# Kernel tuning notes

Hardware: AMD Instinct MI355X
Metric: run time of the kernel (lower is better)

Reference implementation:

```python
import jax, jax.numpy as jnp
import numpy as np

NEG = -1e9


def setup_inputs() -> dict:
    key = jax.random.key(0)
    ks = jax.random.split(key, 5)
    B, N, D = 2, 1024, 40
    x = jax.random.normal(ks[0], (B, N, D), dtype=jnp.float32)
    # Linear(2D->D): store as (2D, D) so y = cat @ W1 + b1 (transposed torch layout)
    W1 = jax.random.normal(ks[1], (2 * D, D), dtype=jnp.float32) * (1.0 / np.sqrt(2 * D))
    b1 = jax.random.normal(ks[2], (D,), dtype=jnp.float32) * 0.01
    W2 = jax.random.normal(ks[3], (D, D), dtype=jnp.float32) * (1.0 / np.sqrt(D))
    b2 = jax.random.normal(ks[4], (D,), dtype=jnp.float32) * 0.01
    return {"x": x, "W1": W1, "b1": b1, "W2": W2, "b2": b2}


def reference(x, W1, b1, W2, b2):
    B, N, D = x.shape
    # cat([xi, xj]) @ W1 == xi @ W1[:D] + xj @ W1[D:] -> avoid (B,N,N,2D) materialization
    ai = x @ W1[:D]          # (B, N, D), contribution of row index i
    aj = x @ W1[D:]          # (B, N, D), contribution of col index j
    h = jax.nn.gelu(ai[:, :, None, :] + aj[:, None, :, :] + b1, approximate=False)  # (B,N,N,D)
    p = h @ W2 + b2          # (B, N, N, D)
    mask = jnp.triu(jnp.ones((N, N), dtype=bool), 1)  # True where j > i (masked out)
    p = jnp.where(mask[None, :, :, None], 0.0, p)
    sq = jnp.sum(p * p, axis=-1)                       # (B, N, N)
    s = jnp.sqrt(jnp.where(mask[None], 1.0, sq))       # safe sqrt at masked zeros
    s = jnp.where(mask[None], NEG, s)
    w = jax.nn.softmax(s, axis=-1)                     # softmax over j
    return jnp.sum(w[..., None] * p, axis=2)           # (B, N, D)
```

## Files before the change

kernel.cpp:

```cpp
#include <hip/hip_runtime.h>
#include <math.h>

#define D 40
#define NN 1024
#define BB 2

typedef __attribute__((ext_vector_type(8))) _Float16 f16x8;
typedef __attribute__((ext_vector_type(4))) float f32x4;

__device__ __forceinline__ unsigned int pk16(float a, float b) {
    return __builtin_bit_cast(unsigned int, __builtin_amdgcn_cvt_pkrtz(a, b));
}

__device__ __forceinline__ float gelu_tanh(float a) {
    float u = a * a;
    float t1 = fmaf(0.10294366f, u, 2.3022083f);
    float e = __builtin_amdgcn_exp2f(a * t1);
    float r = __builtin_amdgcn_rcpf(e + 1.0f);
    return fmaf(-a, r, a);
}

__device__ __forceinline__ void pinf(float& x) { asm volatile("" : "+v"(x)); }
__device__ __forceinline__ void pin4(float4& v) {
    asm volatile("" : "+v"(v.x), "+v"(v.y), "+v"(v.z), "+v"(v.w));
}
__device__ __forceinline__ void pin8(f16x8& v) {
    uint4 u = __builtin_bit_cast(uint4, v);
    asm volatile("" : "+v"(u.x), "+v"(u.y), "+v"(u.z), "+v"(u.w));
    v = __builtin_bit_cast(f16x8, u);
}

__device__ __forceinline__ f16x8 frag8(float4 a0, float4 a1, float4 x0, float4 x1) {
    float g0 = gelu_tanh(a0.x + x0.x);
    float g1 = gelu_tanh(a0.y + x0.y);
    float g2 = gelu_tanh(a0.z + x0.z);
    float g3 = gelu_tanh(a0.w + x0.w);
    float g4 = gelu_tanh(a1.x + x1.x);
    float g5 = gelu_tanh(a1.y + x1.y);
    float g6 = gelu_tanh(a1.z + x1.z);
    float g7 = gelu_tanh(a1.w + x1.w);
    return __builtin_bit_cast(f16x8,
        make_uint4(pk16(g0, g1), pk16(g2, g3), pk16(g4, g5), pk16(g6, g7)));
}

__global__ __launch_bounds__(256) void precompute_kernel(
    const float* __restrict__ x, const float* __restrict__ W1,
    const float* __restrict__ b1, const float* __restrict__ W2,
    float* __restrict__ ai, float* __restrict__ aj, uint4* __restrict__ w2fT) {
    const int t = threadIdx.x;
    const int bid = blockIdx.x;
    const int r = (bid << 1) + (t >> 7);
    const int tl = t & 127;
    const float* xr = x + (size_t)r * D;

    if (tl < D) {
        const int d = tl;
        float s = b1[d];
#pragma unroll
        for (int k = 0; k < D; ++k) s = fmaf(xr[k], W1[k * D + d], s);
        ai[(size_t)r * D + d] = s;
    } else if (tl >= 64 && tl < 64 + D) {
        const int d = tl - 64;
        float s = 0.0f;
#pragma unroll
        for (int k = 0; k < D; ++k) s = fmaf(xr[k], W1[(D + k) * D + d], s);
        aj[(size_t)r * D + d] = s;
    }

    if (bid == 0 && t < 64) {
        const int lr = t & 15, lg = t >> 4;
#pragma unroll
        for (int mt = 0; mt < 3; ++mt)
#pragma unroll
            for (int kt = 0; kt < 2; ++kt) {
                unsigned int u[4];
#pragma unroll
                for (int pe = 0; pe < 4; ++pe) {
                    int k0 = kt * 32 + lg * 8 + pe * 2;
                    int dd = mt * 16 + lr;
                    float v0 = (k0 < D && dd < D) ? W2[k0 * D + dd] : 0.0f;
                    float v1 = (k0 + 1 < D && dd < D) ? W2[(k0 + 1) * D + dd] : 0.0f;
                    u[pe] = pk16(v0, v1);
                }
                w2fT[(mt * 2 + kt) * 64 + t] = make_uint4(u[0], u[1], u[2], u[3]);
            }
    }
}

__global__ __launch_bounds__(256)
__attribute__((amdgpu_waves_per_eu(4)))
void pair_kernel(
    const float* __restrict__ ai_g, const float* __restrict__ aj_g,
    const uint4* __restrict__ w2fT, const float* __restrict__ b2,
    float* __restrict__ out) {
    __shared__ float mbuf[224];

    const int t = threadIdx.x;
    const int bid = blockIdx.x;
    const int bb = bid & 1;
    const int i = NN - 1 - (bid >> 1);
    const int w = t >> 6;
    const int l = t & 63;
    const int lr = l & 15;
    const int lg = l >> 4;

    f16x8 w2t[3][2];
#pragma unroll
    for (int mt = 0; mt < 3; ++mt)
#pragma unroll
        for (int kt = 0; kt < 2; ++kt) {
            w2t[mt][kt] = __builtin_bit_cast(f16x8, w2fT[(mt * 2 + kt) * 64 + l]);
            pin8(w2t[mt][kt]);
        }

    float bv2[3][4];
#pragma unroll
    for (int mt = 0; mt < 3; ++mt)
#pragma unroll
        for (int r = 0; r < 4; ++r) {
            int d = mt * 16 + lg * 4 + r;
            bv2[mt][r] = (d < D) ? b2[d] : 0.0f;
            pinf(bv2[mt][r]);
        }

    const float* ai_row = ai_g + ((size_t)bb * NN + i) * D;
    float4 air0 = *reinterpret_cast<const float4*>(ai_row + (lg << 3));
    float4 air1 = *reinterpret_cast<const float4*>(ai_row + (lg << 3) + 4);
    float4 ai32 = *reinterpret_cast<const float4*>(ai_row + 32 + ((l >> 5) << 2));
    pin4(air0); pin4(air1); pin4(ai32);

    const float* aj_b = aj_g + (size_t)bb * NN * D;

    float m_run = 0.0f, l_run = 0.0f;
    float o[3][4];
#pragma unroll
    for (int mt = 0; mt < 3; ++mt)
#pragma unroll
        for (int r = 0; r < 4; ++r) o[mt][r] = 0.0f;

    const int idxA = lr << 2;

    auto window = [&](int jbase, float4 qa0, float4 qa1, float4 qb0,
                      float4 qb1, float4 qt, bool masked) {
        unsigned int pd0, pd1;
        {
            float g0 = gelu_tanh(ai32.x + qt.x);
            float g1 = gelu_tanh(ai32.y + qt.y);
            float g2 = gelu_tanh(ai32.z + qt.z);
            float g3 = gelu_tanh(ai32.w + qt.w);
            pd0 = pk16(g0, g1);
            pd1 = pk16(g2, g3);
        }
        uint4 tB0, tB1;
        tB0.x = __builtin_amdgcn_ds_bpermute(idxA,       pd0);
        tB0.y = __builtin_amdgcn_ds_bpermute(idxA,       pd1);
        tB0.z = __builtin_amdgcn_ds_bpermute(idxA + 128, pd0);
        tB0.w = __builtin_amdgcn_ds_bpermute(idxA + 128, pd1);
        tB1.x = __builtin_amdgcn_ds_bpermute(idxA + 64,  pd0);
        tB1.y = __builtin_amdgcn_ds_bpermute(idxA + 64,  pd1);
        tB1.z = __builtin_amdgcn_ds_bpermute(idxA + 192, pd0);
        tB1.w = __builtin_amdgcn_ds_bpermute(idxA + 192, pd1);

        f32x4 acc[3][2];
#pragma unroll
        for (int mt = 0; mt < 3; ++mt)
#pragma unroll
            for (int n = 0; n < 2; ++n)
                acc[mt][n] = (f32x4){bv2[mt][0], bv2[mt][1], bv2[mt][2], bv2[mt][3]};
        {
            f16x8 B = frag8(air0, air1, qa0, qa1);
            f16x8 Bt = __builtin_bit_cast(f16x8, tB0);
#pragma unroll
            for (int mt = 0; mt < 3; ++mt) {
                acc[mt][0] = __builtin_amdgcn_mfma_f32_16x16x32_f16(
                    w2t[mt][0], B, acc[mt][0], 0, 0, 0);
                acc[mt][0] = __builtin_amdgcn_mfma_f32_16x16x32_f16(
                    w2t[mt][1], Bt, acc[mt][0], 0, 0, 0);
            }
        }
        {
            f16x8 B = frag8(air0, air1, qb0, qb1);
            f16x8 Bt = __builtin_bit_cast(f16x8, tB1);
#pragma unroll
            for (int mt = 0; mt < 3; ++mt) {
                acc[mt][1] = __builtin_amdgcn_mfma_f32_16x16x32_f16(
                    w2t[mt][0], B, acc[mt][1], 0, 0, 0);
                acc[mt][1] = __builtin_amdgcn_mfma_f32_16x16x32_f16(
                    w2t[mt][1], Bt, acc[mt][1], 0, 0, 0);
            }
        }

        float sv[2];
#pragma unroll
        for (int n = 0; n < 2; ++n) {
            float sq = 0.0f;
#pragma unroll
            for (int mt = 0; mt < 3; ++mt)
#pragma unroll
                for (int r = 0; r < 4; ++r)
                    sq = fmaf(acc[mt][n][r], acc[mt][n][r], sq);
            sq += __shfl_xor(sq, 16);
            sq += __shfl_xor(sq, 32);
            if (masked) {
                int j = jbase + n * 16 + lr;
                sv[n] = (j <= i) ? __builtin_amdgcn_sqrtf(sq) : -1e30f;
            } else {
                sv[n] = __builtin_amdgcn_sqrtf(sq);
            }
        }
        float mx = fmaxf(sv[0], sv[1]);
        mx = fmaxf(mx, __shfl_xor(mx, 1));
        mx = fmaxf(mx, __shfl_xor(mx, 2));
        mx = fmaxf(mx, __shfl_xor(mx, 4));
        mx = fmaxf(mx, __shfl_xor(mx, 8));
        if (mx > m_run) {
            float scale = __expf(m_run - mx);
            l_run *= scale;
#pragma unroll
            for (int mt = 0; mt < 3; ++mt)
#pragma unroll
                for (int r = 0; r < 4; ++r) o[mt][r] *= scale;
            m_run = mx;
        }
        float w0 = __expf(sv[0] - m_run);
        float w1 = __expf(sv[1] - m_run);
        l_run += w0 + w1;
#pragma unroll
        for (int mt = 0; mt < 3; ++mt)
#pragma unroll
            for (int r = 0; r < 4; ++r)
                o[mt][r] = fmaf(w0, acc[mt][0][r], fmaf(w1, acc[mt][1][r], o[mt][r]));
    };

    int jbase = w << 5;
    const float* pA = aj_b + (size_t)(jbase + lr) * D + (lg << 3);
    const float* pT = aj_b + (size_t)(jbase + (l & 31)) * D + 32 + ((l >> 5) << 2);
    for (; jbase + 31 <= i; jbase += 128) {
        float4 qa0 = *reinterpret_cast<const float4*>(pA);
        float4 qa1 = *reinterpret_cast<const float4*>(pA + 4);
        float4 qb0 = *reinterpret_cast<const float4*>(pA + 16 * D);
        float4 qb1 = *reinterpret_cast<const float4*>(pA + 16 * D + 4);
        float4 qt  = *reinterpret_cast<const float4*>(pT);
        pA += 128 * D;
        pT += 128 * D;
        window(jbase, qa0, qa1, qb0, qb1, qt, false);
    }
    if (jbase <= i) {
        const int j0 = min(jbase + lr, i);
        const int j1 = min(jbase + 16 + lr, i);
        const int jt = min(jbase + (l & 31), i);
        const float* r0 = aj_b + (size_t)j0 * D + (lg << 3);
        const float* r1 = aj_b + (size_t)j1 * D + (lg << 3);
        float4 qa0 = *reinterpret_cast<const float4*>(r0);
        float4 qa1 = *reinterpret_cast<const float4*>(r0 + 4);
        float4 qb0 = *reinterpret_cast<const float4*>(r1);
        float4 qb1 = *reinterpret_cast<const float4*>(r1 + 4);
        float4 qt  = *reinterpret_cast<const float4*>(
            aj_b + (size_t)jt * D + 32 + ((l >> 5) << 2));
        window(jbase, qa0, qa1, qb0, qb1, qt, true);
    }

#pragma unroll
    for (int mt = 0; mt < 3; ++mt)
#pragma unroll
        for (int r = 0; r < 4; ++r) {
            float v = o[mt][r];
            v += __shfl_xor(v, 1);
            v += __shfl_xor(v, 2);
            v += __shfl_xor(v, 4);
            v += __shfl_xor(v, 8);
            o[mt][r] = v;
        }
    l_run += __shfl_xor(l_run, 1);
    l_run += __shfl_xor(l_run, 2);
    l_run += __shfl_xor(l_run, 4);
    l_run += __shfl_xor(l_run, 8);

    if (lr == 0) {
#pragma unroll
        for (int mt = 0; mt < 3; ++mt)
#pragma unroll
            for (int r = 0; r < 4; ++r) {
                int d = mt * 16 + lg * 4 + r;
                if (d < D) mbuf[w * 56 + d] = o[mt][r];
            }
        if (lg == 0) { mbuf[w * 56 + 48] = l_run; mbuf[w * 56 + 49] = m_run; }
    }
    __syncthreads();
    if (t < D) {
        float Mg = fmaxf(fmaxf(mbuf[49], mbuf[56 + 49]),
                         fmaxf(mbuf[112 + 49], mbuf[168 + 49]));
        float L = 0.0f, val = 0.0f;
#pragma unroll
        for (int ww = 0; ww < 4; ++ww) {
            float c = __expf(mbuf[ww * 56 + 49] - Mg);
            L = fmaf(c, mbuf[ww * 56 + 48], L);
            val = fmaf(c, mbuf[ww * 56 + t], val);
        }
        out[((size_t)bb * NN + i) * D + t] = val / L;
    }
}

extern "C" void kernel_launch(void* const* d_in, const int* in_sizes, int n_in,
                              void* d_out, int out_size, void* d_ws, size_t ws_size,
                              hipStream_t stream) {
    const float* x  = (const float*)d_in[0];
    const float* W1 = (const float*)d_in[1];
    const float* b1 = (const float*)d_in[2];
    const float* W2 = (const float*)d_in[3];
    const float* b2 = (const float*)d_in[4];
    float* out = (float*)d_out;

    float* ai = (float*)d_ws;
    float* aj = ai + (size_t)BB * NN * D;
    uint4* w2fT = (uint4*)(aj + (size_t)BB * NN * D);

    precompute_kernel<<<BB * NN / 2, 256, 0, stream>>>(x, W1, b1, W2, ai, aj, w2fT);
    pair_kernel<<<BB * NN, 256, 0, stream>>>(ai, aj, w2fT, b2, out);
}
```

Before: 34.90 us.

## Split pair work into balanced fixed-size tasks with partial sums and merge kernel

```diff
diff --git a/kernel.cpp b/kernel.cpp
--- a/kernel.cpp
+++ b/kernel.cpp
@@ -4,6 +4,11 @@
 #define D 40
 #define NN 1024
 #define BB 2
+#define NWPB 4608
+#define NTASK (2*NWPB)
+#define GP 1024
+#define TPB 9
+#define PSTR 44
 
 typedef __attribute__((ext_vector_type(8))) _Float16 f16x8;
 typedef __attribute__((ext_vector_type(4))) float f32x4;
@@ -18,16 +23,6 @@
     float e = __builtin_amdgcn_exp2f(a * t1);
     float r = __builtin_amdgcn_rcpf(e + 1.0f);
     return fmaf(-a, r, a);
-}
-
-__device__ __forceinline__ void pinf(float& x) { asm volatile("" : "+v"(x)); }
-__device__ __forceinline__ void pin4(float4& v) {
-    asm volatile("" : "+v"(v.x), "+v"(v.y), "+v"(v.z), "+v"(v.w));
-}
-__device__ __forceinline__ void pin8(f16x8& v) {
-    uint4 u = __builtin_bit_cast(uint4, v);
-    asm volatile("" : "+v"(u.x), "+v"(u.y), "+v"(u.z), "+v"(u.w));
-    v = __builtin_bit_cast(f16x8, u);
 }
 
 __device__ __forceinline__ f16x8 frag8(float4 a0, float4 a1, float4 x0, float4 x1) {
@@ -87,31 +82,26 @@
     }
 }
 
-__global__ __launch_bounds__(256)
-__attribute__((amdgpu_waves_per_eu(4)))
-void pair_kernel(
+__global__ __launch_bounds__(256) void pair_partial_kernel(
     const float* __restrict__ ai_g, const float* __restrict__ aj_g,
     const uint4* __restrict__ w2fT, const float* __restrict__ b2,
-    float* __restrict__ out) {
+    float* __restrict__ partial) {
     __shared__ float mbuf[224];
 
     const int t = threadIdx.x;
     const int bid = blockIdx.x;
-    const int bb = bid & 1;
-    const int i = NN - 1 - (bid >> 1);
-    const int w = t >> 6;
+    const int wv = t >> 6;
     const int l = t & 63;
     const int lr = l & 15;
     const int lg = l >> 4;
+    const int idxA = lr << 2;
 
     f16x8 w2t[3][2];
 #pragma unroll
     for (int mt = 0; mt < 3; ++mt)
 #pragma unroll
-        for (int kt = 0; kt < 2; ++kt) {
+        for (int kt = 0; kt < 2; ++kt)
             w2t[mt][kt] = __builtin_bit_cast(f16x8, w2fT[(mt * 2 + kt) * 64 + l]);
-            pin8(w2t[mt][kt]);
-        }
 
     float bv2[3][4];
 #pragma unroll
@@ -120,184 +110,191 @@
         for (int r = 0; r < 4; ++r) {
             int d = mt * 16 + lg * 4 + r;
             bv2[mt][r] = (d < D) ? b2[d] : 0.0f;
-            pinf(bv2[mt][r]);
-        }
-
-    const float* ai_row = ai_g + ((size_t)bb * NN + i) * D;
-    float4 air0 = *reinterpret_cast<const float4*>(ai_row + (lg << 3));
-    float4 air1 = *reinterpret_cast<const float4*>(ai_row + (lg << 3) + 4);
-    float4 ai32 = *reinterpret_cast<const float4*>(ai_row + 32 + ((l >> 5) << 2));
-    pin4(air0); pin4(air1); pin4(ai32);
-
-    const float* aj_b = aj_g + (size_t)bb * NN * D;
-
-    float m_run = 0.0f, l_run = 0.0f;
-    float o[3][4];
-#pragma unroll
-    for (int mt = 0; mt < 3; ++mt)
-#pragma unroll
-        for (int r = 0; r < 4; ++r) o[mt][r] = 0.0f;
-
-    const int idxA = lr << 2;
-
-    auto window = [&](int jbase, float4 qa0, float4 qa1, float4 qb0,
-                      float4 qb1, float4 qt, bool masked) {
-        unsigned int pd0, pd1;
-        {
-            float g0 = gelu_tanh(ai32.x + qt.x);
-            float g1 = gelu_tanh(ai32.y + qt.y);
-            float g2 = gelu_tanh(ai32.z + qt.z);
-            float g3 = gelu_tanh(ai32.w + qt.w);
-            pd0 = pk16(g0, g1);
-            pd1 = pk16(g2, g3);
-        }
-        uint4 tB0, tB1;
-        tB0.x = __builtin_amdgcn_ds_bpermute(idxA,       pd0);
-        tB0.y = __builtin_amdgcn_ds_bpermute(idxA,       pd1);
-        tB0.z = __builtin_amdgcn_ds_bpermute(idxA + 128, pd0);
-        tB0.w = __builtin_amdgcn_ds_bpermute(idxA + 128, pd1);
-        tB1.x = __builtin_amdgcn_ds_bpermute(idxA + 64,  pd0);
-        tB1.y = __builtin_amdgcn_ds_bpermute(idxA + 64,  pd1);
-        tB1.z = __builtin_amdgcn_ds_bpermute(idxA + 192, pd0);
-        tB1.w = __builtin_amdgcn_ds_bpermute(idxA + 192, pd1);
-
-        f32x4 acc[3][2];
+        }
+
+    int T0 = bid * TPB;
+    int bb = (T0 >= NWPB) ? 1 : 0;
+    int tp = T0 - bb * NWPB;
+    int g = 0;
+#pragma unroll
+    for (int gg = 1; gg < 8; ++gg)
+        if (tp >= 64 * gg * (gg + 1)) g = gg;
+    const int dd0 = tp - 64 * g * (g + 1);
+    const int ioff = dd0 / (g + 1);
+    int i = (g << 7) + ioff;
+    int w = dd0 - ioff * (g + 1);
+    int nw = g + 1;
+
+    int k = 0;
+    while (k < TPB) {
+        const int run = min(TPB - k, nw - w);
+
+        for (int c = 0; c < run - 1; ++c)
+            if (t < PSTR) partial[(size_t)(T0 + k + c) * PSTR + t] = 0.0f;
+
+        const float* ai_row = ai_g + ((size_t)bb * NN + i) * D;
+        float4 air0 = *reinterpret_cast<const float4*>(ai_row + (lg << 3));
+        float4 air1 = *reinterpret_cast<const float4*>(ai_row + (lg << 3) + 4);
+        float4 ai32 = *reinterpret_cast<const float4*>(ai_row + 32 + ((l >> 5) << 2));
+        const float* aj_b = aj_g + (size_t)bb * NN * D;
+
+        float l_run = 0.0f;
+        float o[3][4];
 #pragma unroll
         for (int mt = 0; mt < 3; ++mt)
 #pragma unroll
-            for (int n = 0; n < 2; ++n)
-                acc[mt][n] = (f32x4){bv2[mt][0], bv2[mt][1], bv2[mt][2], bv2[mt][3]};
-        {
-            f16x8 B = frag8(air0, air1, qa0, qa1);
-            f16x8 Bt = __builtin_bit_cast(f16x8, tB0);
-#pragma unroll
-            for (int mt = 0; mt < 3; ++mt) {
-                acc[mt][0] = __builtin_amdgcn_mfma_f32_16x16x32_f16(
-                    w2t[mt][0], B, acc[mt][0], 0, 0, 0);
-                acc[mt][0] = __builtin_amdgcn_mfma_f32_16x16x32_f16(
-                    w2t[mt][1], Bt, acc[mt][0], 0, 0, 0);
-            }
-        }
-        {
-            f16x8 B = frag8(air0, air1, qb0, qb1);
-            f16x8 Bt = __builtin_bit_cast(f16x8, tB1);
-#pragma unroll
-            for (int mt = 0; mt < 3; ++mt) {
-                acc[mt][1] = __builtin_amdgcn_mfma_f32_16x16x32_f16(
-                    w2t[mt][0], B, acc[mt][1], 0, 0, 0);
-                acc[mt][1] = __builtin_amdgcn_mfma_f32_16x16x32_f16(
-                    w2t[mt][1], Bt, acc[mt][1], 0, 0, 0);
-            }
-        }
-
-        float sv[2];
-#pragma unroll
-        for (int n = 0; n < 2; ++n) {
-            float sq = 0.0f;
+            for (int r = 0; r < 4; ++r) o[mt][r] = 0.0f;
+
+        for (int c = 0; c < run; ++c) {
+            const int jb = ((w + c) << 7) + (wv << 5);
+            const int j0 = min(jb + lr, i);
+            const int j1 = min(jb + 16 + lr, i);
+            const int jt = min(jb + (l & 31), i);
+            const float* r0 = aj_b + (size_t)j0 * D + (lg << 3);
+            const float* r1 = aj_b + (size_t)j1 * D + (lg << 3);
+            float4 qa0 = *reinterpret_cast<const float4*>(r0);
+            float4 qa1 = *reinterpret_cast<const float4*>(r0 + 4);
+            float4 qb0 = *reinterpret_cast<const float4*>(r1);
+            float4 qb1 = *reinterpret_cast<const float4*>(r1 + 4);
+            float4 qt  = *reinterpret_cast<const float4*>(
+                aj_b + (size_t)jt * D + 32 + ((l >> 5) << 2));
+
+            unsigned int pd0, pd1;
+            {
+                float g0 = gelu_tanh(ai32.x + qt.x);
+                float g1 = gelu_tanh(ai32.y + qt.y);
+                float g2 = gelu_tanh(ai32.z + qt.z);
+                float g3 = gelu_tanh(ai32.w + qt.w);
+                pd0 = pk16(g0, g1);
+                pd1 = pk16(g2, g3);
+            }
+            uint4 tB0, tB1;
+            tB0.x = __builtin_amdgcn_ds_bpermute(idxA,       pd0);
+            tB0.y = __builtin_amdgcn_ds_bpermute(idxA,       pd1);
+            tB0.z = __builtin_amdgcn_ds_bpermute(idxA + 128, pd0);
+            tB0.w = __builtin_amdgcn_ds_bpermute(idxA + 128, pd1);
+            tB1.x = __builtin_amdgcn_ds_bpermute(idxA + 64,  pd0);
+            tB1.y = __builtin_amdgcn_ds_bpermute(idxA + 64,  pd1);
+            tB1.z = __builtin_amdgcn_ds_bpermute(idxA + 192, pd0);
+            tB1.w = __builtin_amdgcn_ds_bpermute(idxA + 192, pd1);
+
+            f32x4 acc[3][2];
 #pragma unroll
             for (int mt = 0; mt < 3; ++mt)
 #pragma unroll
+                for (int n = 0; n < 2; ++n)
+                    acc[mt][n] = (f32x4){bv2[mt][0], bv2[mt][1], bv2[mt][2], bv2[mt][3]};
+            {
+                f16x8 B = frag8(air0, air1, qa0, qa1);
+                f16x8 Bt = __builtin_bit_cast(f16x8, tB0);
+#pragma unroll
+                for (int mt = 0; mt < 3; ++mt) {
+                    acc[mt][0] = __builtin_amdgcn_mfma_f32_16x16x32_f16(
+                        w2t[mt][0], B, acc[mt][0], 0, 0, 0);
+                    acc[mt][0] = __builtin_amdgcn_mfma_f32_16x16x32_f16(
+                        w2t[mt][1], Bt, acc[mt][0], 0, 0, 0);
+                }
+            }
+            {
+                f16x8 B = frag8(air0, air1, qb0, qb1);
+                f16x8 Bt = __builtin_bit_cast(f16x8, tB1);
+#pragma unroll
+                for (int mt = 0; mt < 3; ++mt) {
+                    acc[mt][1] = __builtin_amdgcn_mfma_f32_16x16x32_f16(
+                        w2t[mt][0], B, acc[mt][1], 0, 0, 0);
+                    acc[mt][1] = __builtin_amdgcn_mfma_f32_16x16x32_f16(
+                        w2t[mt][1], Bt, acc[mt][1], 0, 0, 0);
+                }
+            }
+
+            float sv[2];
+#pragma unroll
+            for (int n = 0; n < 2; ++n) {
+                float sq = 0.0f;
+#pragma unroll
+                for (int mt = 0; mt < 3; ++mt)
+#pragma unroll
+                    for (int r = 0; r < 4; ++r)
+                        sq = fmaf(acc[mt][n][r], acc[mt][n][r], sq);
+                sq += __shfl_xor(sq, 16);
+                sq += __shfl_xor(sq, 32);
+                int j = jb + n * 16 + lr;
+                sv[n] = (j <= i) ? __builtin_amdgcn_sqrtf(sq) : -1e30f;
+            }
+            float w0 = __expf(sv[0]);
+            float w1 = __expf(sv[1]);
+            l_run += w0 + w1;
+#pragma unroll
+            for (int mt = 0; mt < 3; ++mt)
+#pragma unroll
                 for (int r = 0; r < 4; ++r)
-                    sq = fmaf(acc[mt][n][r], acc[mt][n][r], sq);
-            sq += __shfl_xor(sq, 16);
-            sq += __shfl_xor(sq, 32);
-            if (masked) {
-                int j = jbase + n * 16 + lr;
-                sv[n] = (j <= i) ? __builtin_amdgcn_sqrtf(sq) : -1e30f;
-            } else {
-                sv[n] = __builtin_amdgcn_sqrtf(sq);
-            }
-        }
-        float mx = fmaxf(sv[0], sv[1]);
-        mx = fmaxf(mx, __shfl_xor(mx, 1));
-        mx = fmaxf(mx, __shfl_xor(mx, 2));
-        mx = fmaxf(mx, __shfl_xor(mx, 4));
-        mx = fmaxf(mx, __shfl_xor(mx, 8));
-        if (mx > m_run) {
-            float scale = __expf(m_run - mx);
-            l_run *= scale;
+                    o[mt][r] = fmaf(w0, acc[mt][0][r],
+                                    fmaf(w1, acc[mt][1][r], o[mt][r]));
+        }
+
+#pragma unroll
+        for (int mt = 0; mt < 3; ++mt)
+#pragma unroll
+            for (int r = 0; r < 4; ++r) {
+                float v = o[mt][r];
+                v += __shfl_xor(v, 1);
+                v += __shfl_xor(v, 2);
+                v += __shfl_xor(v, 4);
+                v += __shfl_xor(v, 8);
+                o[mt][r] = v;
+            }
+        l_run += __shfl_xor(l_run, 1);
+        l_run += __shfl_xor(l_run, 2);
+        l_run += __shfl_xor(l_run, 4);
+        l_run += __shfl_xor(l_run, 8);
+
+        __syncthreads();
+        if (lr == 0) {
 #pragma unroll
             for (int mt = 0; mt < 3; ++mt)
 #pragma unroll
-                for (int r = 0; r < 4; ++r) o[mt][r] *= scale;
-            m_run = mx;
-        }
-        float w0 = __expf(sv[0] - m_run);
-        float w1 = __expf(sv[1] - m_run);
-        l_run += w0 + w1;
-#pragma unroll
-        for (int mt = 0; mt < 3; ++mt)
-#pragma unroll
-            for (int r = 0; r < 4; ++r)
-                o[mt][r] = fmaf(w0, acc[mt][0][r], fmaf(w1, acc[mt][1][r], o[mt][r]));
-    };
-
-    int jbase = w << 5;
-    const float* pA = aj_b + (size_t)(jbase + lr) * D + (lg << 3);
-    const float* pT = aj_b + (size_t)(jbase + (l & 31)) * D + 32 + ((l >> 5) << 2);
-    for (; jbase + 31 <= i; jbase += 128) {
-        float4 qa0 = *reinterpret_cast<const float4*>(pA);
-        float4 qa1 = *reinterpret_cast<const float4*>(pA + 4);
-        float4 qb0 = *reinterpret_cast<const float4*>(pA + 16 * D);
-        float4 qb1 = *reinterpret_cast<const float4*>(pA + 16 * D + 4);
-        float4 qt  = *reinterpret_cast<const float4*>(pT);
-        pA += 128 * D;
-        pT += 128 * D;
-        window(jbase, qa0, qa1, qb0, qb1, qt, false);
+                for (int r = 0; r < 4; ++r) {
+                    int d = mt * 16 + lg * 4 + r;
+                    if (d < D) mbuf[wv * 56 + d] = o[mt][r];
+                }
+            if (lg == 0) mbuf[wv * 56 + 48] = l_run;
+        }
+        __syncthreads();
+        if (t < 41) {
+            const int src = (t < 40) ? t : 48;
+            float s = mbuf[src] + mbuf[56 + src] + mbuf[112 + src] + mbuf[168 + src];
+            partial[(size_t)(T0 + k + run - 1) * PSTR + t] = s;
+        }
+
+        k += run;
+        w += run;
+        if (w == nw) {
+            w = 0;
+            ++i;
+            if (i == NN) { i = 0; ++bb; }
+            nw = (i >> 7) + 1;
+        }
     }
-    if (jbase <= i) {
-        const int j0 = min(jbase + lr, i);
-        const int j1 = min(jbase + 16 + lr, i);
-        const int jt = min(jbase + (l & 31), i);
-        const float* r0 = aj_b + (size_t)j0 * D + (lg << 3);
-        const float* r1 = aj_b + (size_t)j1 * D + (lg << 3);
-        float4 qa0 = *reinterpret_cast<const float4*>(r0);
-        float4 qa1 = *reinterpret_cast<const float4*>(r0 + 4);
-        float4 qb0 = *reinterpret_cast<const float4*>(r1);
-        float4 qb1 = *reinterpret_cast<const float4*>(r1 + 4);
-        float4 qt  = *reinterpret_cast<const float4*>(
-            aj_b + (size_t)jt * D + 32 + ((l >> 5) << 2));
-        window(jbase, qa0, qa1, qb0, qb1, qt, true);
-    }
-
-#pragma unroll
-    for (int mt = 0; mt < 3; ++mt)
-#pragma unroll
-        for (int r = 0; r < 4; ++r) {
-            float v = o[mt][r];
-            v += __shfl_xor(v, 1);
-            v += __shfl_xor(v, 2);
-            v += __shfl_xor(v, 4);
-            v += __shfl_xor(v, 8);
-            o[mt][r] = v;
-        }
-    l_run += __shfl_xor(l_run, 1);
-    l_run += __shfl_xor(l_run, 2);
-    l_run += __shfl_xor(l_run, 4);
-    l_run += __shfl_xor(l_run, 8);
-
-    if (lr == 0) {
-#pragma unroll
-        for (int mt = 0; mt < 3; ++mt)
-#pragma unroll
-            for (int r = 0; r < 4; ++r) {
-                int d = mt * 16 + lg * 4 + r;
-                if (d < D) mbuf[w * 56 + d] = o[mt][r];
-            }
-        if (lg == 0) { mbuf[w * 56 + 48] = l_run; mbuf[w * 56 + 49] = m_run; }
-    }
-    __syncthreads();
+}
+
+__global__ __launch_bounds__(64) void merge_kernel(
+    const float* __restrict__ partial, float* __restrict__ out) {
+    const int row = blockIdx.x;
+    const int bb = row >> 10;
+    const int i = row & (NN - 1);
+    const int g = i >> 7;
+    const int nw = g + 1;
+    const int base = ((g * (g + 1)) << 6) + (i & 127) * nw;
+    const int T0 = bb * NWPB + base;
+    const int t = threadIdx.x;
     if (t < D) {
-        float Mg = fmaxf(fmaxf(mbuf[49], mbuf[56 + 49]),
-                         fmaxf(mbuf[112 + 49], mbuf[168 + 49]));
-        float L = 0.0f, val = 0.0f;
-#pragma unroll
-        for (int ww = 0; ww < 4; ++ww) {
-            float c = __expf(mbuf[ww * 56 + 49] - Mg);
-            L = fmaf(c, mbuf[ww * 56 + 48], L);
-            val = fmaf(c, mbuf[ww * 56 + t], val);
-        }
-        out[((size_t)bb * NN + i) * D + t] = val / L;
+        float val = 0.0f, L = 0.0f;
+        for (int w = 0; w < nw; ++w) {
+            const float* P = partial + (size_t)(T0 + w) * PSTR;
+            val += P[t];
+            L += P[40];
+        }
+        out[(size_t)row * D + t] = val / L;
     }
 }
 
@@ -314,7 +311,9 @@
     float* ai = (float*)d_ws;
     float* aj = ai + (size_t)BB * NN * D;
     uint4* w2fT = (uint4*)(aj + (size_t)BB * NN * D);
+    float* partial = (float*)(w2fT + 384);
 
     precompute_kernel<<<BB * NN / 2, 256, 0, stream>>>(x, W1, b1, W2, ai, aj, w2fT);
-    pair_kernel<<<BB * NN, 256, 0, stream>>>(ai, aj, w2fT, b2, out);
-}
+    pair_partial_kernel<<<GP, 256, 0, stream>>>(ai, aj, w2fT, b2, partial);
+    merge_kernel<<<BB * NN, 64, 0, stream>>>(partial, out);
+}
```

Result: slower. 46.86 us (+34.3%).
